# Kernel optimization log

Hardware: AMD Instinct MI355X
Metric: run time of the kernel (lower is better)

## Reference

```python
import jax, jax.numpy as jnp
import numpy as np

TOPK = 13
NUM_CLASSES = 80
ALPHA = 1.0
BETA = 6.0
EPS = 1e-9
IMG = 640.0


def setup_inputs() -> dict:
    key = jax.random.key(0)
    k = jax.random.split(key, 8)
    bs, A, C, n = 32, 8400, NUM_CLASSES, 64
    pd_scores = jax.random.uniform(k[0], (bs, A, C), dtype=jnp.float32)
    # valid x1y1x2y2 predicted boxes
    ctr = jax.random.uniform(k[1], (bs, A, 2), dtype=jnp.float32) * IMG
    wh = jax.random.uniform(k[2], (bs, A, 2), dtype=jnp.float32) * 90.0 + 10.0
    pd_bboxes = jnp.concatenate([ctr - wh / 2, ctr + wh / 2], axis=-1)
    anc_points = jax.random.uniform(k[3], (8400, 2), dtype=jnp.float32) * IMG
    gt_labels = jax.random.randint(k[4], (bs, n, 1), 0, C, dtype=jnp.int64)
    gctr = jax.random.uniform(k[5], (bs, n, 2), dtype=jnp.float32) * IMG
    gwh = jax.random.uniform(k[6], (bs, n, 2), dtype=jnp.float32) * 140.0 + 20.0
    gt_bboxes = jnp.concatenate([gctr - gwh / 2, gctr + gwh / 2], axis=-1)
    mask_gt = (jax.random.uniform(k[7], (bs, n, 1)) < 0.8).astype(jnp.float32)
    return {"pd_scores": pd_scores, "pd_bboxes": pd_bboxes, "anc_points": anc_points,
            "gt_labels": gt_labels, "gt_bboxes": gt_bboxes, "mask_gt": mask_gt}


def _assign(pd_scores, pd_bboxes, anc_points, gt_labels, gt_bboxes, mask_gt):
    b, A, C = pd_scores.shape
    n = gt_bboxes.shape[1]
    gl = gt_labels.reshape(b, n).astype(jnp.int32)

    # bbox_scores[b,n,a] = pd_scores[b, a, gt_labels[b,n]]  -> (b, n, A)
    bbox_scores = jnp.take_along_axis(pd_scores.transpose(0, 2, 1), gl[:, :, None], axis=1)

    # pairwise IoU: gt (b,n,1,4) vs pred (b,1,A,4) -> (b,n,A)
    b1 = gt_bboxes[:, :, None, :]
    b2 = pd_bboxes[:, None, :, :]
    lt = jnp.maximum(b1[..., :2], b2[..., :2])
    rb = jnp.minimum(b1[..., 2:], b2[..., 2:])
    overlap = jnp.clip(rb - lt, 0).prod(-1)
    area1 = jnp.clip(b1[..., 2:] - b1[..., :2], 0).prod(-1)
    area2 = jnp.clip(b2[..., 2:] - b2[..., :2], 0).prod(-1)
    overlaps = overlap / (area1 + area2 - overlap + EPS)

    align_metric = (bbox_scores ** ALPHA) * (overlaps ** BETA)

    # anchor centers inside gt boxes -> (b,n,A)
    lt_d = anc_points[None, None, :, :] - gt_bboxes[:, :, None, :2]
    rb_d = gt_bboxes[:, :, None, 2:] - anc_points[None, None, :, :]
    deltas = jnp.concatenate([lt_d, rb_d], axis=-1)
    mask_in_gts = (deltas.min(-1) > EPS).astype(gt_bboxes.dtype)

    # topk candidate selection with scatter-count (avoids (b,n,topk,A) one-hot)
    metrics = align_metric * mask_in_gts
    _, topk_idxs = jax.lax.top_k(metrics, TOPK)  # (b,n,TOPK)
    topk_mask = mask_gt.reshape(b, n, 1) != 0
    topk_idxs = jnp.where(topk_mask, topk_idxs, 0)
    bi = jnp.arange(b)[:, None, None]
    ni = jnp.arange(n)[None, :, None]
    counts = jnp.zeros((b, n, A), jnp.int32).at[bi, ni, topk_idxs].add(1)
    is_in_topk = jnp.where(counts > 1, 0, counts).astype(metrics.dtype)

    mask_pos = is_in_topk * mask_in_gts * mask_gt.reshape(b, n, 1)

    # resolve anchors assigned to multiple gts by highest IoU
    fg_mask = mask_pos.sum(-2)                         # (b,A)
    mask_multi = fg_mask[:, None, :] > 1               # (b,1,A) broadcast over n
    max_idx = overlaps.argmax(axis=1)                  # (b,A)
    is_max = jax.nn.one_hot(max_idx, n, dtype=overlaps.dtype).transpose(0, 2, 1)  # (b,n,A)
    mask_pos = jnp.where(mask_multi, is_max, mask_pos)
    fg_mask = mask_pos.sum(-2)
    target_gt_idx = mask_pos.argmax(-2)                # (b,A)

    # gather targets
    target_labels = jnp.take_along_axis(gl, target_gt_idx, axis=1)            # (b,A)
    target_labels = jnp.maximum(target_labels, 0)
    target_bboxes = jnp.take_along_axis(gt_bboxes, target_gt_idx[:, :, None], axis=1)  # (b,A,4)
    target_scores = jax.nn.one_hot(target_labels, C, dtype=pd_scores.dtype)
    target_scores = jnp.where(fg_mask[:, :, None] > 0, target_scores, 0.0)

    # normalize scores by alignment metric
    align_metric = align_metric * mask_pos
    pos_align = align_metric.max(-1, keepdims=True)                  # (b,n,1)
    pos_overlaps = (overlaps * mask_pos).max(-1, keepdims=True)      # (b,n,1)
    norm = (align_metric * pos_overlaps / (pos_align + EPS)).max(-2)[:, :, None]  # (b,A,1)
    target_scores = target_scores * norm

    return target_labels, target_bboxes, target_scores, fg_mask > 0


def reference(pd_scores, pd_bboxes, anc_points, gt_labels, gt_bboxes, mask_gt):
    return _assign(pd_scores, pd_bboxes, anc_points, gt_labels, gt_bboxes, mask_gt)
```

## Files before the change

kernel.cpp:

```cpp
#include <hip/hip_runtime.h>
#include <math.h>

#define A_N   8400
#define BS    32
#define NGT   64
#define NC    80
#define TK    13
#define EPSF  1e-9f
#define CAP   1024
#define JG    32
#define NJG   2
#define NTILE 33
#define PCAP  64
#define NCAND (BS * NTILE * NJG)

typedef float nt4 __attribute__((ext_vector_type(4)));

#define OFF_LB 0
#define OFF_BB (BS * A_N)
#define OFF_SC (OFF_BB + BS * A_N * 4)
#define OFF_FG (OFF_SC + BS * A_N * NC)

#define WS_FLAG   0
#define WS_CNT    256
#define WS_MINJ   (WS_CNT   + BS * A_N * 4)
#define WS_INFO   (WS_MINJ  + BS * A_N * 4)
#define WS_ALIGN  (WS_INFO  + BS * A_N * 4)
#define WS_POSA   (WS_ALIGN + BS * A_N * 4)
#define WS_POSO   (WS_POSA  + BS * NGT * 4)
#define WS_CNT2   (WS_POSO  + BS * NGT * 4)
#define WS_CAND   (WS_CNT2  + BS * NGT * 4)

__device__ __forceinline__ float iou_f(float g0, float g1, float g2, float g3,
                                       float p0, float p1, float p2, float p3) {
    float ltx = fmaxf(g0, p0), lty = fmaxf(g1, p1);
    float rbx = fminf(g2, p2), rby = fminf(g3, p3);
    float ov  = fmaxf(rbx - ltx, 0.f) * fmaxf(rby - lty, 0.f);
    float a1  = fmaxf(g2 - g0, 0.f) * fmaxf(g3 - g1, 0.f);
    float a2  = fmaxf(p2 - p0, 0.f) * fmaxf(p3 - p1, 0.f);
    return ov / (a1 + a2 - ov + EPSF);
}

__device__ __forceinline__ int get_gl(const int* g, int flag64, int i) {
    return flag64 ? g[2 * i] : g[i];
}

__device__ __forceinline__ unsigned long long shfl_xor_u64(unsigned long long x, int m) {
    int lo = __shfl_xor((int)(unsigned int)(x & 0xFFFFFFFFull), m, 64);
    int hi = __shfl_xor((int)(unsigned int)(x >> 32), m, 64);
    return ((unsigned long long)(unsigned int)hi << 32) | (unsigned int)lo;
}

__global__ __launch_bounds__(256) void k_init(unsigned int* posA, unsigned int* posO,
                                              int* cnt2, int* flag, const int* gl_raw) {
    int i = blockIdx.x * 256 + threadIdx.x;
    if (i < BS * NGT) { posA[i] = 0u; posO[i] = 0u; cnt2[i] = 0; }
    if (i == 0) {
        int f = 1;
        for (int k = 0; k < 64; k++) {
            if (gl_raw[2 * k + 1] != 0) { f = 0; break; }
        }
        *flag = f;
    }
}

__global__ __launch_bounds__(256) void k_cand(
    const float* __restrict__ pd_scores, const float* __restrict__ pd_bboxes,
    const float* __restrict__ anc, const int* __restrict__ gl_raw,
    const float* __restrict__ gt_bboxes, const float* __restrict__ mask_gt,
    const int* __restrict__ flag,
    int* __restrict__ cnt2, unsigned long long* __restrict__ cand,
    int* __restrict__ cnt, int* __restrict__ minj, float* __restrict__ out) {
    __shared__ float4 sgt[JG];
    __shared__ int    slbl[JG];
    __shared__ int    smask[JG];
    __shared__ int    cnt_lds[JG];
    __shared__ int    base_lds[JG];
    __shared__ unsigned long long pool[JG][PCAP];

    int bid  = blockIdx.x;
    int b    = bid / (NTILE * NJG);
    int rem  = bid % (NTILE * NJG);
    int tile = rem / NJG;
    int jg   = rem % NJG;
    int tid  = threadIdx.x;
    int a    = tile * 256 + tid;
    int jbase = b * NGT + jg * JG;

    if (tid < JG) {
        sgt[tid]   = ((const float4*)gt_bboxes)[jbase + tid];
        slbl[tid]  = get_gl(gl_raw, *flag, jbase + tid);
        smask[tid] = (mask_gt[jbase + tid] != 0.f);
        cnt_lds[tid] = 0;
    }
    __syncthreads();

    bool act = (a < A_N);
    float2 an = make_float2(0.f, 0.f);
    float4 p  = make_float4(0.f, 0.f, 0.f, 0.f);
    const float* sc = pd_scores;
    if (act) {
        an = ((const float2*)anc)[a];
        p  = ((const float4*)pd_bboxes)[(size_t)b * A_N + a];
        sc = pd_scores + (size_t)b * A_N * NC + (size_t)a * NC;
    }

    for (int j = 0; j < JG; j++) {
        if (!smask[j]) continue;
        if (!act) continue;
        float4 g = sgt[j];
        float d = fminf(fminf(an.x - g.x, an.y - g.y),
                        fminf(g.z - an.x, g.w - an.y));
        if (d > EPSF) {
            float iou = iou_f(g.x, g.y, g.z, g.w, p.x, p.y, p.z, p.w);
            float m = 0.f;
            if (iou > 0.f) {
                float s = sc[slbl[j]];
                m = s * powf(iou, 6.0f);
            }
            unsigned long long key =
                ((unsigned long long)__float_as_uint(m) << 32) |
                (unsigned int)(~(unsigned int)a);
            int slot = atomicAdd(&cnt_lds[j], 1);
            if (slot < PCAP) {
                pool[j][slot] = key;
            } else {
                int gs = atomicAdd(&cnt2[jbase + j], 1);
                if (gs < CAP) cand[(size_t)(jbase + j) * CAP + gs] = key;
            }
        }
    }
    __syncthreads();

    if (tid < JG) {
        int c = min(cnt_lds[tid], PCAP);
        int bas = 0;
        if (c > 0) bas = atomicAdd(&cnt2[jbase + tid], c);
        base_lds[tid] = bas;
    }
    __syncthreads();

    for (int j = 0; j < JG; j++) {
        int c = min(cnt_lds[j], PCAP);
        int bas = base_lds[j];
        for (int t = tid; t < c; t += 256) {
            int dst = bas + t;
            if (dst < CAP) cand[(size_t)(jbase + j) * CAP + dst] = pool[j][t];
        }
    }

    {
        int gth = bid * 256 + tid;
        const int GS = NCAND * 256;
        nt4* scz = (nt4*)(out + OFF_SC);
        for (int t = gth; t < BS * A_N * (NC / 4); t += GS)
            __builtin_nontemporal_store((nt4)(0.f), &scz[t]);
        for (int t = gth; t < BS * A_N; t += GS) {
            cnt[t] = 0; minj[t] = 1 << 30;
        }
    }
}

template <int NT>
__device__ __forceinline__ void pick_body(
    int lane, int b, int j, int n, const unsigned long long* __restrict__ L,
    int* __restrict__ cnt, int* __restrict__ minj) {
    unsigned long long k0[NT];
    #pragma unroll
    for (int t = 0; t < NT; t++) {
        int i = t * 64 + lane;
        k0[t] = (i < n) ? L[i] : 0ULL;
    }

    unsigned int wanchor[TK];
    int P = 0;
    #pragma unroll
    for (int r = 0; r < TK; r++) {
        unsigned long long best = 0;
        #pragma unroll
        for (int t = 0; t < NT; t++) best = (k0[t] > best) ? k0[t] : best;
        for (int s = 1; s < 64; s <<= 1) {
            unsigned long long o = shfl_xor_u64(best, s);
            if (o > best) best = o;
        }
        if (!(best >> 32)) break;
        unsigned int aw = ~(unsigned int)(best & 0xFFFFFFFFull);
        wanchor[r] = aw;
        if (lane == 0) {
            atomicAdd(&cnt[b * A_N + (int)aw], 1);
            atomicMin(&minj[b * A_N + (int)aw], j);
        }
        #pragma unroll
        for (int t = 0; t < NT; t++) if (k0[t] == best) k0[t] = 0;
        P++;
    }

    if (P < TK) {
        int K = TK - P;
        #pragma unroll
        for (int t = 0; t < NT; t++) {
            unsigned long long key = k0[t];
            if (key != 0 && !(key >> 32)) {
                unsigned int a0 = ~(unsigned int)(key & 0xFFFFFFFFull);
                int off = 0;
                #pragma unroll
                for (int r = 0; r < TK; r++)
                    if (r < P && wanchor[r] < a0) off++;
                if ((int)a0 < K + off) {
                    atomicAdd(&cnt[b * A_N + (int)a0], 1);
                    atomicMin(&minj[b * A_N + (int)a0], j);
                }
            }
        }
    }
}

__global__ __launch_bounds__(256) void k_pick(
    const int* __restrict__ cnt2, const unsigned long long* __restrict__ cand,
    int* __restrict__ cnt, int* __restrict__ minj) {
    int lane = threadIdx.x & 63;
    int wave = threadIdx.x >> 6;
    int bj = blockIdx.x * 4 + wave;
    int b = bj >> 6, j = bj & 63;

    int n = min(cnt2[bj], CAP);
    if (n == 0) return;
    const unsigned long long* L = cand + (size_t)bj * CAP;

    if (n <= 128)      pick_body<2>(lane, b, j, n, L, cnt, minj);
    else if (n <= 320) pick_body<5>(lane, b, j, n, L, cnt, minj);
    else               pick_body<16>(lane, b, j, n, L, cnt, minj);
}

__global__ __launch_bounds__(256) void k_assign(
    const float* __restrict__ pd_scores, const float* __restrict__ pd_bboxes,
    const float* __restrict__ gt_bboxes, const int* __restrict__ gl_raw,
    const int* __restrict__ flag,
    const int* __restrict__ cnt, const int* __restrict__ minj,
    int* __restrict__ info, float* __restrict__ alignArr,
    unsigned int* posA, unsigned int* posO, float* __restrict__ out) {
    int i = blockIdx.x * 256 + threadIdx.x;
    if (i >= BS * A_N) return;
    int b = i / A_N;
    int c = cnt[i];
    int f64 = *flag;

    float4 p = ((const float4*)pd_bboxes)[i];
    int jstar = 0;
    if (c == 1) {
        jstar = minj[i];
    } else if (c > 1) {
        float bv = -1.f; int bj_ = 0;
        const float4* gb = (const float4*)(gt_bboxes + (size_t)b * NGT * 4);
        for (int j = 0; j < NGT; j++) {
            float4 g = gb[j];
            float ov = iou_f(g.x, g.y, g.z, g.w, p.x, p.y, p.z, p.w);
            if (ov > bv) { bv = ov; bj_ = j; }
        }
        jstar = bj_;
    }

    int lbl = get_gl(gl_raw, f64, b * NGT + jstar);
    if (lbl < 0) lbl = 0;

    out[OFF_LB + i] = (float)lbl;
    float4 g = ((const float4*)gt_bboxes)[b * NGT + jstar];
    ((float4*)(out + OFF_BB))[i] = g;

    int fg = (c > 0) ? 1 : 0;
    out[OFF_FG + i] = (float)fg;

    float al = 0.f;
    if (fg) {
        float ov = iou_f(g.x, g.y, g.z, g.w, p.x, p.y, p.z, p.w);
        float s  = pd_scores[(size_t)i * NC + lbl];
        al = s * powf(ov, 6.0f);
        atomicMax((int*)&posA[b * NGT + jstar], __float_as_int(al));
        atomicMax((int*)&posO[b * NGT + jstar], __float_as_int(ov));
    }
    alignArr[i] = al;
    info[i] = jstar | (lbl << 8) | (fg << 16);
}

__global__ __launch_bounds__(256) void k_norm(
    const int* __restrict__ info, const float* __restrict__ alignArr,
    const unsigned int* __restrict__ posA, const unsigned int* __restrict__ posO,
    float* __restrict__ out) {
    int i = blockIdx.x * 256 + threadIdx.x;
    if (i >= BS * A_N) return;
    int inf = info[i];
    if (!(inf & (1 << 16))) return;
    int jstar = inf & 255;
    int lbl   = (inf >> 8) & 255;
    int b = i / A_N;
    float pa = __int_as_float((int)posA[b * NGT + jstar]);
    float po = __int_as_float((int)posO[b * NGT + jstar]);
    out[OFF_SC + (size_t)i * NC + lbl] = alignArr[i] * po / (pa + EPSF);
}

extern "C" void kernel_launch(void* const* d_in, const int* in_sizes, int n_in,
                              void* d_out, int out_size, void* d_ws, size_t ws_size,
                              hipStream_t stream) {
    const float* pd_scores = (const float*)d_in[0];
    const float* pd_bboxes = (const float*)d_in[1];
    const float* anc       = (const float*)d_in[2];
    const int*   gl_raw    = (const int*)d_in[3];
    const float* gt_bboxes = (const float*)d_in[4];
    const float* mask_gt   = (const float*)d_in[5];
    float* out = (float*)d_out;

    char* ws = (char*)d_ws;
    int*                flag     = (int*)(ws + WS_FLAG);
    int*                cnt      = (int*)(ws + WS_CNT);
    int*                minj     = (int*)(ws + WS_MINJ);
    int*                info     = (int*)(ws + WS_INFO);
    float*              alignArr = (float*)(ws + WS_ALIGN);
    unsigned int*       posA     = (unsigned int*)(ws + WS_POSA);
    unsigned int*       posO     = (unsigned int*)(ws + WS_POSO);
    int*                cnt2     = (int*)(ws + WS_CNT2);
    unsigned long long* cand     = (unsigned long long*)(ws + WS_CAND);

    k_init<<<8, 256, 0, stream>>>(posA, posO, cnt2, flag, gl_raw);
    k_cand<<<NCAND, 256, 0, stream>>>(pd_scores, pd_bboxes, anc, gl_raw,
                                      gt_bboxes, mask_gt, flag, cnt2, cand,
                                      cnt, minj, out);
    k_pick<<<BS * NGT / 4, 256, 0, stream>>>(cnt2, cand, cnt, minj);
    k_assign<<<(BS * A_N + 255) / 256, 256, 0, stream>>>(pd_scores, pd_bboxes, gt_bboxes,
                                                         gl_raw, flag, cnt, minj,
                                                         info, alignArr, posA, posO, out);
    k_norm<<<(BS * A_N + 255) / 256, 256, 0, stream>>>(info, alignArr, posA, posO, out);
}
```

Baseline: 210.3 us.

## Fuse pick, assign and norm kernels into one persistent kernel with grid barriers

Merges the three tail kernels into a single persistent kernel of 768 blocks that uses global atomic-counter barriers between phases, removing two kernel launch gaps. It also changes the gt grouping in the candidate kernel from 2 groups of 32 to 4 groups of 16, which doubles its block count. The grid barrier relies on all 768 blocks being co-resident, so it could deadlock if occupancy is too low, and the spin-waiting adds latency of its own.

```diff
diff --git a/kernel.cpp b/kernel.cpp
--- a/kernel.cpp
+++ b/kernel.cpp
@@ -8,11 +8,12 @@
 #define TK    13
 #define EPSF  1e-9f
 #define CAP   1024
-#define JG    32
-#define NJG   2
+#define JG    16
+#define NJG   4
 #define NTILE 33
 #define PCAP  64
 #define NCAND (BS * NTILE * NJG)
+#define NBLK_TAIL 768
 
 typedef float nt4 __attribute__((ext_vector_type(4)));
 
@@ -51,10 +52,24 @@
     return ((unsigned long long)(unsigned int)hi << 32) | (unsigned int)lo;
 }
 
+__device__ __forceinline__ void gbar(int* ctr, int nblk) {
+    __syncthreads();
+    __threadfence();
+    if (threadIdx.x == 0) {
+        __hip_atomic_fetch_add(ctr, 1, __ATOMIC_ACQ_REL, __HIP_MEMORY_SCOPE_AGENT);
+        while (__hip_atomic_load(ctr, __ATOMIC_ACQUIRE, __HIP_MEMORY_SCOPE_AGENT) < nblk)
+            __builtin_amdgcn_s_sleep(1);
+    }
+    __syncthreads();
+    __threadfence();
+}
+
 __global__ __launch_bounds__(256) void k_init(unsigned int* posA, unsigned int* posO,
-                                              int* cnt2, int* flag, const int* gl_raw) {
+                                              int* cnt2, int* flag, int* bar,
+                                              const int* gl_raw) {
     int i = blockIdx.x * 256 + threadIdx.x;
     if (i < BS * NGT) { posA[i] = 0u; posO[i] = 0u; cnt2[i] = 0; }
+    if (i == 1 || i == 2) bar[i - 1] = 0;
     if (i == 0) {
         int f = 1;
         for (int k = 0; k < 64; k++) {
@@ -215,87 +230,84 @@
     }
 }
 
-__global__ __launch_bounds__(256) void k_pick(
-    const int* __restrict__ cnt2, const unsigned long long* __restrict__ cand,
-    int* __restrict__ cnt, int* __restrict__ minj) {
-    int lane = threadIdx.x & 63;
-    int wave = threadIdx.x >> 6;
-    int bj = blockIdx.x * 4 + wave;
-    int b = bj >> 6, j = bj & 63;
-
-    int n = min(cnt2[bj], CAP);
-    if (n == 0) return;
-    const unsigned long long* L = cand + (size_t)bj * CAP;
-
-    if (n <= 128)      pick_body<2>(lane, b, j, n, L, cnt, minj);
-    else if (n <= 320) pick_body<5>(lane, b, j, n, L, cnt, minj);
-    else               pick_body<16>(lane, b, j, n, L, cnt, minj);
-}
-
-__global__ __launch_bounds__(256) void k_assign(
+__global__ __launch_bounds__(256, 4) void k_tail(
     const float* __restrict__ pd_scores, const float* __restrict__ pd_bboxes,
     const float* __restrict__ gt_bboxes, const int* __restrict__ gl_raw,
     const int* __restrict__ flag,
-    const int* __restrict__ cnt, const int* __restrict__ minj,
+    const int* __restrict__ cnt2, const unsigned long long* __restrict__ cand,
+    int* __restrict__ cnt, int* __restrict__ minj,
     int* __restrict__ info, float* __restrict__ alignArr,
-    unsigned int* posA, unsigned int* posO, float* __restrict__ out) {
-    int i = blockIdx.x * 256 + threadIdx.x;
-    if (i >= BS * A_N) return;
-    int b = i / A_N;
-    int c = cnt[i];
-    int f64 = *flag;
-
-    float4 p = ((const float4*)pd_bboxes)[i];
-    int jstar = 0;
-    if (c == 1) {
-        jstar = minj[i];
-    } else if (c > 1) {
-        float bv = -1.f; int bj_ = 0;
-        const float4* gb = (const float4*)(gt_bboxes + (size_t)b * NGT * 4);
-        for (int j = 0; j < NGT; j++) {
-            float4 g = gb[j];
+    unsigned int* posA, unsigned int* posO,
+    int* __restrict__ bar, float* __restrict__ out) {
+    int tid  = threadIdx.x;
+    int lane = tid & 63;
+    int f64  = *flag;
+
+    for (int bj = blockIdx.x * 4 + (tid >> 6); bj < BS * NGT; bj += NBLK_TAIL * 4) {
+        int n = min(cnt2[bj], CAP);
+        if (n == 0) continue;
+        int b = bj >> 6, j = bj & 63;
+        const unsigned long long* L = cand + (size_t)bj * CAP;
+        if (n <= 128)      pick_body<2>(lane, b, j, n, L, cnt, minj);
+        else if (n <= 320) pick_body<5>(lane, b, j, n, L, cnt, minj);
+        else               pick_body<16>(lane, b, j, n, L, cnt, minj);
+    }
+
+    gbar(&bar[0], NBLK_TAIL);
+
+    for (int i = blockIdx.x * 256 + tid; i < BS * A_N; i += NBLK_TAIL * 256) {
+        int b = i / A_N;
+        int c = cnt[i];
+
+        float4 p = ((const float4*)pd_bboxes)[i];
+        int jstar = 0;
+        if (c == 1) {
+            jstar = minj[i];
+        } else if (c > 1) {
+            float bv = -1.f; int bj_ = 0;
+            const float4* gb = (const float4*)(gt_bboxes + (size_t)b * NGT * 4);
+            for (int j = 0; j < NGT; j++) {
+                float4 g = gb[j];
+                float ov = iou_f(g.x, g.y, g.z, g.w, p.x, p.y, p.z, p.w);
+                if (ov > bv) { bv = ov; bj_ = j; }
+            }
+            jstar = bj_;
+        }
+
+        int lbl = get_gl(gl_raw, f64, b * NGT + jstar);
+        if (lbl < 0) lbl = 0;
+
+        out[OFF_LB + i] = (float)lbl;
+        float4 g = ((const float4*)gt_bboxes)[b * NGT + jstar];
+        ((float4*)(out + OFF_BB))[i] = g;
+
+        int fg = (c > 0) ? 1 : 0;
+        out[OFF_FG + i] = (float)fg;
+
+        float al = 0.f;
+        if (fg) {
             float ov = iou_f(g.x, g.y, g.z, g.w, p.x, p.y, p.z, p.w);
-            if (ov > bv) { bv = ov; bj_ = j; }
-        }
-        jstar = bj_;
-    }
-
-    int lbl = get_gl(gl_raw, f64, b * NGT + jstar);
-    if (lbl < 0) lbl = 0;
-
-    out[OFF_LB + i] = (float)lbl;
-    float4 g = ((const float4*)gt_bboxes)[b * NGT + jstar];
-    ((float4*)(out + OFF_BB))[i] = g;
-
-    int fg = (c > 0) ? 1 : 0;
-    out[OFF_FG + i] = (float)fg;
-
-    float al = 0.f;
-    if (fg) {
-        float ov = iou_f(g.x, g.y, g.z, g.w, p.x, p.y, p.z, p.w);
-        float s  = pd_scores[(size_t)i * NC + lbl];
-        al = s * powf(ov, 6.0f);
-        atomicMax((int*)&posA[b * NGT + jstar], __float_as_int(al));
-        atomicMax((int*)&posO[b * NGT + jstar], __float_as_int(ov));
-    }
-    alignArr[i] = al;
-    info[i] = jstar | (lbl << 8) | (fg << 16);
-}
-
-__global__ __launch_bounds__(256) void k_norm(
-    const int* __restrict__ info, const float* __restrict__ alignArr,
-    const unsigned int* __restrict__ posA, const unsigned int* __restrict__ posO,
-    float* __restrict__ out) {
-    int i = blockIdx.x * 256 + threadIdx.x;
-    if (i >= BS * A_N) return;
-    int inf = info[i];
-    if (!(inf & (1 << 16))) return;
-    int jstar = inf & 255;
-    int lbl   = (inf >> 8) & 255;
-    int b = i / A_N;
-    float pa = __int_as_float((int)posA[b * NGT + jstar]);
-    float po = __int_as_float((int)posO[b * NGT + jstar]);
-    out[OFF_SC + (size_t)i * NC + lbl] = alignArr[i] * po / (pa + EPSF);
+            float s  = pd_scores[(size_t)i * NC + lbl];
+            al = s * powf(ov, 6.0f);
+            atomicMax((int*)&posA[b * NGT + jstar], __float_as_int(al));
+            atomicMax((int*)&posO[b * NGT + jstar], __float_as_int(ov));
+        }
+        alignArr[i] = al;
+        info[i] = jstar | (lbl << 8) | (fg << 16);
+    }
+
+    gbar(&bar[1], NBLK_TAIL);
+
+    for (int i = blockIdx.x * 256 + tid; i < BS * A_N; i += NBLK_TAIL * 256) {
+        int inf = info[i];
+        if (!(inf & (1 << 16))) continue;
+        int jstar = inf & 255;
+        int lbl   = (inf >> 8) & 255;
+        int b = i / A_N;
+        float pa = __int_as_float((int)posA[b * NGT + jstar]);
+        float po = __int_as_float((int)posO[b * NGT + jstar]);
+        out[OFF_SC + (size_t)i * NC + lbl] = alignArr[i] * po / (pa + EPSF);
+    }
 }
 
 extern "C" void kernel_launch(void* const* d_in, const int* in_sizes, int n_in,
@@ -311,6 +323,7 @@
 
     char* ws = (char*)d_ws;
     int*                flag     = (int*)(ws + WS_FLAG);
+    int*                bar      = (int*)(ws + WS_FLAG + 16);
     int*                cnt      = (int*)(ws + WS_CNT);
     int*                minj     = (int*)(ws + WS_MINJ);
     int*                info     = (int*)(ws + WS_INFO);
@@ -320,13 +333,11 @@
     int*                cnt2     = (int*)(ws + WS_CNT2);
     unsigned long long* cand     = (unsigned long long*)(ws + WS_CAND);
 
-    k_init<<<8, 256, 0, stream>>>(posA, posO, cnt2, flag, gl_raw);
+    k_init<<<8, 256, 0, stream>>>(posA, posO, cnt2, flag, bar, gl_raw);
     k_cand<<<NCAND, 256, 0, stream>>>(pd_scores, pd_bboxes, anc, gl_raw,
                                       gt_bboxes, mask_gt, flag, cnt2, cand,
                                       cnt, minj, out);
-    k_pick<<<BS * NGT / 4, 256, 0, stream>>>(cnt2, cand, cnt, minj);
-    k_assign<<<(BS * A_N + 255) / 256, 256, 0, stream>>>(pd_scores, pd_bboxes, gt_bboxes,
-                                                         gl_raw, flag, cnt, minj,
-                                                         info, alignArr, posA, posO, out);
-    k_norm<<<(BS * A_N + 255) / 256, 256, 0, stream>>>(info, alignArr, posA, posO, out);
-}
+    k_tail<<<NBLK_TAIL, 256, 0, stream>>>(pd_scores, pd_bboxes, gt_bboxes, gl_raw,
+                                          flag, cnt2, cand, cnt, minj,
+                                          info, alignArr, posA, posO, bar, out);
+}
```

Measured after the change: 700.5 us. 233% more time.
